# Kernel tuning notes

Measured on AMD Instinct MI355X. Metric: run time of the kernel, lower is better.

Reference implementation:

```python
import jax, jax.numpy as jnp
import numpy as np

S, B, D, N, DH = 1024, 2, 1024, 16, 64  # seq, batch, d_model, n_head, d_head
EPS = 1e-5


def setup_inputs() -> dict:
    key = jax.random.key(0)
    k0, k1, k2, k3 = jax.random.split(key, 4)
    h = jax.random.normal(k0, (S, B, D), dtype=jnp.float32)
    Wq = jax.random.normal(k1, (N * DH, D), dtype=jnp.float32) * 0.02
    Wkv = jax.random.normal(k2, (2 * N * DH, D), dtype=jnp.float32) * 0.02
    Wo = jax.random.normal(k3, (D, N * DH), dtype=jnp.float32) * 0.02
    gamma = jnp.ones((D,), dtype=jnp.float32)
    beta = jnp.zeros((D,), dtype=jnp.float32)
    return {"h": h, "Wq": Wq, "Wkv": Wkv, "Wo": Wo, "gamma": gamma, "beta": beta}


def reference(h, Wq, Wkv, Wo, gamma, beta):
    scale = 1.0 / np.sqrt(DH).astype(np.float32)
    # projections (torch Linear: x @ W.T), no mems so c == h
    q = (h @ Wq.T).reshape(S, B, N, DH)
    kv = h @ Wkv.T                      # [S,B,2*N*DH]
    k, v = jnp.split(kv, 2, axis=-1)
    k = k.reshape(S, B, N, DH)
    v = v.reshape(S, B, N, DH)
    # full attention scores [i,j,b,n]
    score = jnp.einsum('ibnd,jbnd->ijbn', q, k) * scale
    prob = jax.nn.softmax(score, axis=1)  # softmax over keys j
    # twicing correction (layer_num >= 14): P <- 2P - P @ P per (b,n)
    p = prob.transpose(2, 3, 0, 1)       # [b,n,i,j]
    p = 2.0 * p - jnp.matmul(p, p)
    prob = p.transpose(2, 3, 0, 1)       # back to [i,j,b,n]
    # attention output
    vec = jnp.einsum('ijbn,jbnd->ibnd', prob, v).reshape(S, B, N * DH)
    attn_out = vec @ Wo.T                # [S,B,D]
    # post-LN residual
    x = h + attn_out
    mu = jnp.mean(x, axis=-1, keepdims=True)
    var = jnp.mean(jnp.square(x - mu), axis=-1, keepdims=True)
    return (x - mu) / jnp.sqrt(var + EPS) * gamma + beta
```

## Files before the change

### kernel.cpp

```cpp
#include <hip/hip_runtime.h>

typedef unsigned short u16;
typedef unsigned int u32;
typedef __attribute__((ext_vector_type(8))) short short8;
typedef __attribute__((ext_vector_type(4))) float f32x4;

constexpr int kN = 16, kDH = 64, kD = 1024;
constexpr float kEps = 1e-5f;

__device__ __forceinline__ u16 f2b(float f) {
  u32 u = __float_as_uint(f);
  u += 0x7fffu + ((u >> 16) & 1u);
  return (u16)(u >> 16);
}
__device__ __forceinline__ float b2f(u32 bits) {
  return __uint_as_float(bits << 16);
}

__device__ __forceinline__ void gload16(const u16* g, u16* l) {
  __builtin_amdgcn_global_load_lds(
      (const __attribute__((address_space(1))) void*)g,
      (__attribute__((address_space(3))) void*)l, 16, 0, 0);
}

__device__ __forceinline__ short8 read8sw(const u16* base, int row, int colel) {
  return *(const short8*)(base + (row << 6) + (colel ^ ((row & 7) << 3)));
}

__global__ __launch_bounds__(256) void cvt_all(const float* __restrict__ h,
                                               const float* __restrict__ wq,
                                               const float* __restrict__ wkv,
                                               const float* __restrict__ wo,
                                               u16* __restrict__ hb, u16* __restrict__ wqb,
                                               u16* __restrict__ wkvb, u16* __restrict__ wob) {
  long idx = (long)blockIdx.x * 256 + threadIdx.x;
  const float* in;
  u16* out;
  long base;
  if (idx < 524288L) { in = h; out = hb; base = idx; }
  else if (idx < 786432L) { in = wq; out = wqb; base = idx - 524288L; }
  else if (idx < 1310720L) { in = wkv; out = wkvb; base = idx - 786432L; }
  else { in = wo; out = wob; base = idx - 1310720L; }
  float4 v = *(const float4*)(in + base * 4);
  uint2 o;
  o.x = (u32)f2b(v.x) | ((u32)f2b(v.y) << 16);
  o.y = (u32)f2b(v.z) | ((u32)f2b(v.w) << 16);
  *(uint2*)(out + base * 4) = o;
}

struct GemmParams {
  const u16* A; long ldA;
  const u16* B; long ldB;
  const u16* B2;
  int K;
  u16* ob; float* of; long ldO;
  u16* ob2;
  u16* aux_b16;
};

template <int MODE, int BM, int BN, int WC, int MF, int NF>
__global__ __launch_bounds__(256) void gemm_tile(GemmParams p) {
  __shared__ __align__(16) u16 sm[2][(BM + BN) * 32];
  const u16* A = p.A;
  const int tid = threadIdx.x;
  const int lane = tid & 63;
  const int w = tid >> 6;
  const int wR = w / WC, wC = w % WC;
  const int lr = lane & 15, lk = lane >> 4;
  const int bm0 = blockIdx.y * BM, bn0 = blockIdx.x * BN;
  const int m0 = bm0 + wR * (MF * 16), n0 = bn0 + wC * (NF * 16);
  const u16* B = (MODE == 6 && bn0 >= 1024) ? (p.B2 - 1048576) : p.B;

  f32x4 acc[MF][NF];
#pragma unroll
  for (int i = 0; i < MF; ++i)
#pragma unroll
    for (int j = 0; j < NF; ++j) acc[i][j] = (f32x4){0.f, 0.f, 0.f, 0.f};

  constexpr int ACH = BM * 4;
  constexpr int NCH = (BM + BN) * 4;
  constexpr int NLD = NCH / 256;

  auto stage = [&](int k0, int buf) {
#pragma unroll
    for (int i = 0; i < NLD; ++i) {
      const int cbase = i * 256 + w * 64;
      const int c = cbase + lane;
      const u16* g;
      if (cbase < ACH) {
        g = A + (long)(bm0 + (c >> 2)) * p.ldA + k0 + (c & 3) * 8;
      } else {
        const int cc = c - ACH;
        g = B + (long)(bn0 + (cc >> 2)) * p.ldB + k0 + (cc & 3) * 8;
      }
      gload16(g, &sm[buf][cbase * 8]);
    }
  };

  auto compute = [&](int buf) {
    const u16* As = sm[buf];
    const u16* Bs = sm[buf] + BM * 32;
    short8 af[MF], bf[NF];
#pragma unroll
    for (int mi = 0; mi < MF; ++mi)
      af[mi] = *(const short8*)(As + ((wR * MF + mi) * 16 + lr) * 32 + lk * 8);
#pragma unroll
    for (int ni = 0; ni < NF; ++ni)
      bf[ni] = *(const short8*)(Bs + ((wC * NF + ni) * 16 + lr) * 32 + lk * 8);
#pragma unroll
    for (int mi = 0; mi < MF; ++mi)
#pragma unroll
      for (int ni = 0; ni < NF; ++ni)
        acc[mi][ni] = __builtin_amdgcn_mfma_f32_16x16x32_bf16(af[mi], bf[ni], acc[mi][ni], 0, 0, 0);
  };

  const int nt = p.K / 32;
  stage(0, 0);
  __syncthreads();
  for (int t = 0; t < nt - 1; ++t) {
    stage((t + 1) * 32, (t & 1) ^ 1);
    compute(t & 1);
    __syncthreads();
  }
  compute((nt - 1) & 1);

#pragma unroll
  for (int mi = 0; mi < MF; ++mi)
#pragma unroll
    for (int ni = 0; ni < NF; ++ni)
#pragma unroll
      for (int r = 0; r < 4; ++r) {
        int row = m0 + mi * 16 + lk * 4 + r;
        int col = n0 + ni * 16 + lr;
        float v = acc[mi][ni][r];
        if constexpr (MODE == 6) {
          if (col < 1024) {
            p.ob[(long)row * 1024 + col] = f2b(v);
          } else if (col < 2048) {
            p.ob2[(long)row * 1024 + (col - 1024)] = f2b(v);
          } else {
            int c = col - 2048, n = c >> 6, dd = c & 63, s = row >> 1, b = row & 1;
            p.aux_b16[(((long)((b * kN + n) * kDH + dd)) << 10) + s] = f2b(v);
          }
        } else {
          p.of[(long)row * p.ldO + col] = v;
        }
      }
}

template <bool SECOND>
__global__ __launch_bounds__(256) void flash_tw(const u16* __restrict__ qp,
                                                const u16* __restrict__ kp,
                                                const u16* __restrict__ bp,
                                                float* __restrict__ linv_g,
                                                u16* __restrict__ outp) {
  __shared__ __align__(16) u16 Qs[64 * 64];
  __shared__ __align__(16) u16 Ks[2][64 * 64];
  __shared__ __align__(16) u16 Bs[2][64 * 64];
  __shared__ __align__(16) u16 Ss[64 * 64];
  const int z = blockIdx.y;
  const int qb0 = blockIdx.x * 64;
  const int tid = threadIdx.x, lane = tid & 63, w = tid >> 6;
  const int lr = lane & 15, lk = lane >> 4;
  const int wR = w >> 1, wC = w & 1;

#pragma unroll
  for (int i = 0; i < 2; ++i) {
    int c = i * 256 + w * 64 + lane;
    int row = c >> 3, col = (c & 7) ^ (row & 7);
    gload16(qp + (long)(qb0 + row) * 2048 + z * 64 + col * 8, Qs + c * 8);
  }
  auto stageKB = [&](int j, int buf) {
#pragma unroll
    for (int i = 0; i < 2; ++i) {
      int c = i * 256 + w * 64 + lane;
      int row = c >> 3, col = (c & 7) ^ (row & 7);
      gload16(kp + (long)(j * 64 + row) * 2048 + z * 64 + col * 8, Ks[buf] + c * 8);
      gload16(bp + (long)z * 65536 + (long)row * 1024 + j * 64 + col * 8, Bs[buf] + c * 8);
    }
  };
  stageKB(0, 0);
  __syncthreads();

  short8 qf[2][2];
#pragma unroll
  for (int qi = 0; qi < 2; ++qi)
#pragma unroll
    for (int kk = 0; kk < 2; ++kk)
      qf[qi][kk] = read8sw(Qs, wC * 32 + qi * 16 + lr, kk * 32 + lk * 8);

  f32x4 acc[2][2];
#pragma unroll
  for (int i = 0; i < 2; ++i)
#pragma unroll
    for (int j = 0; j < 2; ++j) acc[i][j] = (f32x4){0.f, 0.f, 0.f, 0.f};
  float lsum[2] = {0.f, 0.f};

  for (int j = 0; j < 16; ++j) {
    const int cur = j & 1;
    if (j < 15) stageKB(j + 1, cur ^ 1);
    f32x4 st[2][2];
#pragma unroll
    for (int a = 0; a < 2; ++a)
#pragma unroll
      for (int b = 0; b < 2; ++b) st[a][b] = (f32x4){0.f, 0.f, 0.f, 0.f};
#pragma unroll
    for (int kk = 0; kk < 2; ++kk)
#pragma unroll
      for (int ki = 0; ki < 2; ++ki) {
        short8 kf = read8sw(Ks[cur], wR * 32 + ki * 16 + lr, kk * 32 + lk * 8);
#pragma unroll
        for (int qi = 0; qi < 2; ++qi)
          st[ki][qi] = __builtin_amdgcn_mfma_f32_16x16x32_bf16(kf, qf[qi][kk], st[ki][qi], 0, 0, 0);
      }
#pragma unroll
    for (int ki = 0; ki < 2; ++ki)
#pragma unroll
      for (int qi = 0; qi < 2; ++qi) {
        float e0 = __expf(st[ki][qi][0] * 0.125f);
        float e1 = __expf(st[ki][qi][1] * 0.125f);
        float e2 = __expf(st[ki][qi][2] * 0.125f);
        float e3 = __expf(st[ki][qi][3] * 0.125f);
        if (!SECOND) lsum[qi] += e0 + e1 + e2 + e3;
        int q = wC * 32 + qi * 16 + lr;
        int k0 = wR * 32 + ki * 16 + lk * 4;
        uint2 pk;
        pk.x = (u32)f2b(e0) | ((u32)f2b(e1) << 16);
        pk.y = (u32)f2b(e2) | ((u32)f2b(e3) << 16);
        *(uint2*)(Ss + ((q << 6) + (k0 ^ ((q & 7) << 3)))) = pk;
      }
    __syncthreads();
#pragma unroll
    for (int kk = 0; kk < 2; ++kk) {
      short8 sf0 = read8sw(Ss, wR * 32 + lr, kk * 32 + lk * 8);
      short8 sf1 = read8sw(Ss, wR * 32 + 16 + lr, kk * 32 + lk * 8);
      short8 bf0 = read8sw(Bs[cur], wC * 32 + lr, kk * 32 + lk * 8);
      short8 bf1 = read8sw(Bs[cur], wC * 32 + 16 + lr, kk * 32 + lk * 8);
      acc[0][0] = __builtin_amdgcn_mfma_f32_16x16x32_bf16(sf0, bf0, acc[0][0], 0, 0, 0);
      acc[0][1] = __builtin_amdgcn_mfma_f32_16x16x32_bf16(sf0, bf1, acc[0][1], 0, 0, 0);
      acc[1][0] = __builtin_amdgcn_mfma_f32_16x16x32_bf16(sf1, bf0, acc[1][0], 0, 0, 0);
      acc[1][1] = __builtin_amdgcn_mfma_f32_16x16x32_bf16(sf1, bf1, acc[1][1], 0, 0, 0);
    }
    __syncthreads();
  }

  float* lred = (float*)Ss;
  if (!SECOND) {
#pragma unroll
    for (int qi = 0; qi < 2; ++qi) {
      lsum[qi] += __shfl_xor(lsum[qi], 16);
      lsum[qi] += __shfl_xor(lsum[qi], 32);
      if (lane < 16) lred[wR * 64 + wC * 32 + qi * 16 + lr] = lsum[qi];
    }
    __syncthreads();
    if (tid < 64) {
      float inv = 1.f / (lred[tid] + lred[64 + tid]);
      lred[128 + tid] = inv;
      linv_g[(long)z * 1024 + qb0 + tid] = inv;
    }
    __syncthreads();
  }

#pragma unroll
  for (int qi = 0; qi < 2; ++qi) {
    const int q0 = wR * 32 + qi * 16 + lk * 4;
#pragma unroll
    for (int ni = 0; ni < 2; ++ni) {
      const int d = wC * 32 + ni * 16 + lr;
      if (!SECOND) {
        const float* linv_s = lred + 128;
        u32 lo = (u32)f2b(acc[qi][ni][0] * linv_s[q0]) | ((u32)f2b(acc[qi][ni][1] * linv_s[q0 + 1]) << 16);
        u32 hi = (u32)f2b(acc[qi][ni][2] * linv_s[q0 + 2]) | ((u32)f2b(acc[qi][ni][3] * linv_s[q0 + 3]) << 16);
        uint2 pk; pk.x = lo; pk.y = hi;
        *(uint2*)(outp + (long)z * 65536 + (long)d * 1024 + qb0 + q0) = pk;
      } else {
        float4 l4 = *(const float4*)(linv_g + (long)z * 1024 + qb0 + q0);
        uint2 ut = *(const uint2*)(bp + (long)z * 65536 + (long)d * 1024 + qb0 + q0);
        float u0 = b2f(ut.x & 0xffffu), u1 = b2f(ut.x >> 16);
        float u2 = b2f(ut.y & 0xffffu), u3 = b2f(ut.y >> 16);
        long ob = (long)(qb0 + q0) * 2048 + z * 64 + d;
        outp[ob]        = f2b(2.f * u0 - acc[qi][ni][0] * l4.x);
        outp[ob + 2048] = f2b(2.f * u1 - acc[qi][ni][1] * l4.y);
        outp[ob + 4096] = f2b(2.f * u2 - acc[qi][ni][2] * l4.z);
        outp[ob + 6144] = f2b(2.f * u3 - acc[qi][ni][3] * l4.w);
      }
    }
  }
}

__global__ __launch_bounds__(256) void resid_ln(const float* __restrict__ h,
                                                const float* __restrict__ attn,
                                                const float* __restrict__ gamma,
                                                const float* __restrict__ beta,
                                                float* __restrict__ out) {
  __shared__ float rs[4], rs2[4];
  const long row = blockIdx.x;
  const int t = threadIdx.x;
  long base = (row << 10) + t * 4;
  float4 hv = *(const float4*)(h + base);
  float4 av = *(const float4*)(attn + base);
  float x0 = hv.x + av.x, x1 = hv.y + av.y, x2 = hv.z + av.z, x3 = hv.w + av.w;
  float s = x0 + x1 + x2 + x3;
  float s2 = x0 * x0 + x1 * x1 + x2 * x2 + x3 * x3;
  for (int o = 32; o; o >>= 1) { s += __shfl_xor(s, o); s2 += __shfl_xor(s2, o); }
  int wid = t >> 6;
  if ((t & 63) == 0) { rs[wid] = s; rs2[wid] = s2; }
  __syncthreads();
  s = rs[0] + rs[1] + rs[2] + rs[3];
  s2 = rs2[0] + rs2[1] + rs2[2] + rs2[3];
  float mean = s * (1.f / 1024.f);
  float var = s2 * (1.f / 1024.f) - mean * mean;
  float rstd = rsqrtf(var + kEps);
  int d = t * 4;
  float4 g = *(const float4*)(gamma + d);
  float4 bt = *(const float4*)(beta + d);
  float4 o_;
  o_.x = (x0 - mean) * rstd * g.x + bt.x;
  o_.y = (x1 - mean) * rstd * g.y + bt.y;
  o_.z = (x2 - mean) * rstd * g.z + bt.z;
  o_.w = (x3 - mean) * rstd * g.w + bt.w;
  *(float4*)(out + base) = o_;
}

extern "C" void kernel_launch(void* const* d_in, const int* in_sizes, int n_in,
                              void* d_out, int out_size, void* d_ws, size_t ws_size,
                              hipStream_t stream) {
  const float* h = (const float*)d_in[0];
  const float* Wq = (const float*)d_in[1];
  const float* Wkv = (const float*)d_in[2];
  const float* Wo = (const float*)d_in[3];
  const float* gamma = (const float*)d_in[4];
  const float* beta = (const float*)d_in[5];
  float* out = (float*)d_out;

  char* ws = (char*)d_ws;
  size_t off = 0;
  auto alloc = [&](size_t bytes) -> void* {
    void* p = ws + off;
    off = (off + bytes + 255) & ~(size_t)255;
    return p;
  };
  u16* hb = (u16*)alloc(2097152ULL * 2);
  u16* Wqb = (u16*)alloc(1048576ULL * 2);
  u16* Wkvb = (u16*)alloc(2097152ULL * 2);
  u16* Wob = (u16*)alloc(1048576ULL * 2);
  u16* qb = (u16*)alloc(2097152ULL * 2);
  u16* kb = (u16*)alloc(2097152ULL * 2);
  u16* vtb = (u16*)alloc(2097152ULL * 2);
  u16* Ut = (u16*)alloc(2097152ULL * 2);
  float* linv = (float*)alloc(32768ULL * 4);
  u16* vecb = (u16*)alloc(2097152ULL * 2);
  float* attn = (float*)alloc(2097152ULL * 4);
  (void)ws_size; (void)n_in; (void)in_sizes; (void)out_size;

  cvt_all<<<6144, 256, 0, stream>>>(h, Wq, Wkv, Wo, hb, Wqb, Wkvb, Wob);

  {
    GemmParams p{};
    p.A = hb; p.ldA = 1024;
    p.B = Wqb; p.ldB = 1024; p.B2 = Wkvb;
    p.K = 1024; p.ob = qb; p.ob2 = kb; p.aux_b16 = vtb;
    gemm_tile<6, 64, 64, 2, 2, 2><<<dim3(48, 32, 1), 256, 0, stream>>>(p);
  }
  flash_tw<false><<<dim3(16, 32), 256, 0, stream>>>(qb, kb, vtb, linv, Ut);
  flash_tw<true><<<dim3(16, 32), 256, 0, stream>>>(qb, kb, Ut, linv, vecb);
  {
    GemmParams p{};
    p.A = vecb; p.ldA = 1024;
    p.B = Wob; p.ldB = 1024;
    p.K = 1024; p.of = attn; p.ldO = 1024;
    gemm_tile<5, 64, 64, 2, 2, 2><<<dim3(16, 32, 1), 256, 0, stream>>>(p);
  }
  resid_ln<<<2048, 256, 0, stream>>>(h, attn, gamma, beta, out);
}
```

Measured before the change: 110.4 us.

## Fuse twicing flash passes via cooperative grid sync; widen GEMM K-tile to 64

After: 188.5 us. +70.7%, slower.

```diff
diff --git a/kernel.cpp b/kernel.cpp
--- a/kernel.cpp
+++ b/kernel.cpp
@@ -1,4 +1,7 @@
 #include <hip/hip_runtime.h>
+#include <hip/hip_cooperative_groups.h>
+
+namespace cg = cooperative_groups;
 
 typedef unsigned short u16;
 typedef unsigned int u32;
@@ -58,76 +61,69 @@
   u16* aux_b16;
 };
 
-template <int MODE, int BM, int BN, int WC, int MF, int NF>
+template <int MODE>
 __global__ __launch_bounds__(256) void gemm_tile(GemmParams p) {
-  __shared__ __align__(16) u16 sm[2][(BM + BN) * 32];
+  __shared__ __align__(16) u16 sm[2][8192];
+  const int tid = threadIdx.x, lane = tid & 63, w = tid >> 6;
+  const int wR = w >> 1, wC = w & 1;
+  const int lr = lane & 15, lk = lane >> 4;
+  const int bm0 = blockIdx.y * 64, bn0 = blockIdx.x * 64;
+  const int m0 = bm0 + wR * 32, n0 = bn0 + wC * 32;
   const u16* A = p.A;
-  const int tid = threadIdx.x;
-  const int lane = tid & 63;
-  const int w = tid >> 6;
-  const int wR = w / WC, wC = w % WC;
-  const int lr = lane & 15, lk = lane >> 4;
-  const int bm0 = blockIdx.y * BM, bn0 = blockIdx.x * BN;
-  const int m0 = bm0 + wR * (MF * 16), n0 = bn0 + wC * (NF * 16);
   const u16* B = (MODE == 6 && bn0 >= 1024) ? (p.B2 - 1048576) : p.B;
 
-  f32x4 acc[MF][NF];
-#pragma unroll
-  for (int i = 0; i < MF; ++i)
-#pragma unroll
-    for (int j = 0; j < NF; ++j) acc[i][j] = (f32x4){0.f, 0.f, 0.f, 0.f};
-
-  constexpr int ACH = BM * 4;
-  constexpr int NCH = (BM + BN) * 4;
-  constexpr int NLD = NCH / 256;
+  f32x4 acc[2][2] = {};
 
   auto stage = [&](int k0, int buf) {
 #pragma unroll
-    for (int i = 0; i < NLD; ++i) {
+    for (int i = 0; i < 4; ++i) {
       const int cbase = i * 256 + w * 64;
       const int c = cbase + lane;
       const u16* g;
-      if (cbase < ACH) {
-        g = A + (long)(bm0 + (c >> 2)) * p.ldA + k0 + (c & 3) * 8;
+      if (cbase < 512) {
+        g = A + (long)(bm0 + (c >> 3)) * p.ldA + k0 + (c & 7) * 8;
       } else {
-        const int cc = c - ACH;
-        g = B + (long)(bn0 + (cc >> 2)) * p.ldB + k0 + (cc & 3) * 8;
+        const int cc = c - 512;
+        g = B + (long)(bn0 + (cc >> 3)) * p.ldB + k0 + (cc & 7) * 8;
       }
-      gload16(g, &sm[buf][cbase * 8]);
+      gload16(g, &sm[buf][(size_t)c * 8]);
     }
   };
 
   auto compute = [&](int buf) {
     const u16* As = sm[buf];
-    const u16* Bs = sm[buf] + BM * 32;
-    short8 af[MF], bf[NF];
-#pragma unroll
-    for (int mi = 0; mi < MF; ++mi)
-      af[mi] = *(const short8*)(As + ((wR * MF + mi) * 16 + lr) * 32 + lk * 8);
-#pragma unroll
-    for (int ni = 0; ni < NF; ++ni)
-      bf[ni] = *(const short8*)(Bs + ((wC * NF + ni) * 16 + lr) * 32 + lk * 8);
-#pragma unroll
-    for (int mi = 0; mi < MF; ++mi)
-#pragma unroll
-      for (int ni = 0; ni < NF; ++ni)
-        acc[mi][ni] = __builtin_amdgcn_mfma_f32_16x16x32_bf16(af[mi], bf[ni], acc[mi][ni], 0, 0, 0);
+    const u16* Bs = sm[buf] + 4096;
+    short8 af[2][2], bf[2][2];
+#pragma unroll
+    for (int mi = 0; mi < 2; ++mi)
+#pragma unroll
+      for (int kk = 0; kk < 2; ++kk) {
+        af[mi][kk] = *(const short8*)(As + ((wR * 2 + mi) * 16 + lr) * 64 + kk * 32 + lk * 8);
+        bf[mi][kk] = *(const short8*)(Bs + ((wC * 2 + mi) * 16 + lr) * 64 + kk * 32 + lk * 8);
+      }
+#pragma unroll
+    for (int kk = 0; kk < 2; ++kk)
+#pragma unroll
+      for (int mi = 0; mi < 2; ++mi)
+#pragma unroll
+        for (int ni = 0; ni < 2; ++ni)
+          acc[mi][ni] = __builtin_amdgcn_mfma_f32_16x16x32_bf16(af[mi][kk], bf[ni][kk], acc[mi][ni], 0, 0, 0);
   };
 
-  const int nt = p.K / 32;
+  const int nt = p.K / 64;
   stage(0, 0);
   __syncthreads();
   for (int t = 0; t < nt - 1; ++t) {
-    stage((t + 1) * 32, (t & 1) ^ 1);
+    stage((t + 1) * 64, (t & 1) ^ 1);
     compute(t & 1);
     __syncthreads();
   }
   compute((nt - 1) & 1);
 
 #pragma unroll
-  for (int mi = 0; mi < MF; ++mi)
-#pragma unroll
-    for (int ni = 0; ni < NF; ++ni)
+  for (int mi = 0; mi < 2; ++mi)
+#pragma unroll
+    for (int ni = 0; ni < 2; ++ni)
 #pragma unroll
       for (int r = 0; r < 4; ++r) {
         int row = m0 + mi * 16 + lk * 4 + r;
@@ -148,35 +144,37 @@
       }
 }
 
-template <bool SECOND>
-__global__ __launch_bounds__(256) void flash_tw(const u16* __restrict__ qp,
-                                                const u16* __restrict__ kp,
-                                                const u16* __restrict__ bp,
-                                                float* __restrict__ linv_g,
-                                                u16* __restrict__ outp) {
-  __shared__ __align__(16) u16 Qs[64 * 64];
-  __shared__ __align__(16) u16 Ks[2][64 * 64];
-  __shared__ __align__(16) u16 Bs[2][64 * 64];
-  __shared__ __align__(16) u16 Ss[64 * 64];
-  const int z = blockIdx.y;
-  const int qb0 = blockIdx.x * 64;
-  const int tid = threadIdx.x, lane = tid & 63, w = tid >> 6;
-  const int lr = lane & 15, lk = lane >> 4;
-  const int wR = w >> 1, wC = w & 1;
-
+struct FlashSmem {
+  alignas(16) u16 Qs[64 * 64];
+  alignas(16) u16 Ks[2][64 * 64];
+  alignas(16) u16 Bs[2][64 * 64];
+  alignas(16) u16 Ss[64 * 64];
+};
+
+__device__ __forceinline__ void flash_stage_q(FlashSmem* sm, const u16* qp, int z, int qb0) {
+  const int tid = threadIdx.x, lane = tid & 63, w = tid >> 6;
 #pragma unroll
   for (int i = 0; i < 2; ++i) {
     int c = i * 256 + w * 64 + lane;
     int row = c >> 3, col = (c & 7) ^ (row & 7);
-    gload16(qp + (long)(qb0 + row) * 2048 + z * 64 + col * 8, Qs + c * 8);
-  }
+    gload16(qp + (long)(qb0 + row) * 2048 + z * 64 + col * 8, sm->Qs + c * 8);
+  }
+}
+
+template <bool DO_LSUM>
+__device__ __forceinline__ void flash_core(FlashSmem* sm, const u16* kp, const u16* bp,
+                                           int z, int qb0, f32x4 acc[2][2], float lsum[2]) {
+  const int tid = threadIdx.x, lane = tid & 63, w = tid >> 6;
+  const int lr = lane & 15, lk = lane >> 4;
+  const int wR = w >> 1, wC = w & 1;
+
   auto stageKB = [&](int j, int buf) {
 #pragma unroll
     for (int i = 0; i < 2; ++i) {
       int c = i * 256 + w * 64 + lane;
       int row = c >> 3, col = (c & 7) ^ (row & 7);
-      gload16(kp + (long)(j * 64 + row) * 2048 + z * 64 + col * 8, Ks[buf] + c * 8);
-      gload16(bp + (long)z * 65536 + (long)row * 1024 + j * 64 + col * 8, Bs[buf] + c * 8);
+      gload16(kp + (long)(j * 64 + row) * 2048 + z * 64 + col * 8, sm->Ks[buf] + c * 8);
+      gload16(bp + (long)z * 65536 + (long)row * 1024 + j * 64 + col * 8, sm->Bs[buf] + c * 8);
     }
   };
   stageKB(0, 0);
@@ -187,14 +185,7 @@
   for (int qi = 0; qi < 2; ++qi)
 #pragma unroll
     for (int kk = 0; kk < 2; ++kk)
-      qf[qi][kk] = read8sw(Qs, wC * 32 + qi * 16 + lr, kk * 32 + lk * 8);
-
-  f32x4 acc[2][2];
-#pragma unroll
-  for (int i = 0; i < 2; ++i)
-#pragma unroll
-    for (int j = 0; j < 2; ++j) acc[i][j] = (f32x4){0.f, 0.f, 0.f, 0.f};
-  float lsum[2] = {0.f, 0.f};
+      qf[qi][kk] = read8sw(sm->Qs, wC * 32 + qi * 16 + lr, kk * 32 + lk * 8);
 
   for (int j = 0; j < 16; ++j) {
     const int cur = j & 1;
@@ -208,7 +199,7 @@
     for (int kk = 0; kk < 2; ++kk)
 #pragma unroll
       for (int ki = 0; ki < 2; ++ki) {
-        short8 kf = read8sw(Ks[cur], wR * 32 + ki * 16 + lr, kk * 32 + lk * 8);
+        short8 kf = read8sw(sm->Ks[cur], wR * 32 + ki * 16 + lr, kk * 32 + lk * 8);
 #pragma unroll
         for (int qi = 0; qi < 2; ++qi)
           st[ki][qi] = __builtin_amdgcn_mfma_f32_16x16x32_bf16(kf, qf[qi][kk], st[ki][qi], 0, 0, 0);
@@ -221,21 +212,21 @@
         float e1 = __expf(st[ki][qi][1] * 0.125f);
         float e2 = __expf(st[ki][qi][2] * 0.125f);
         float e3 = __expf(st[ki][qi][3] * 0.125f);
-        if (!SECOND) lsum[qi] += e0 + e1 + e2 + e3;
+        if (DO_LSUM) lsum[qi] += e0 + e1 + e2 + e3;
         int q = wC * 32 + qi * 16 + lr;
         int k0 = wR * 32 + ki * 16 + lk * 4;
         uint2 pk;
         pk.x = (u32)f2b(e0) | ((u32)f2b(e1) << 16);
         pk.y = (u32)f2b(e2) | ((u32)f2b(e3) << 16);
-        *(uint2*)(Ss + ((q << 6) + (k0 ^ ((q & 7) << 3)))) = pk;
+        *(uint2*)(sm->Ss + ((q << 6) + (k0 ^ ((q & 7) << 3)))) = pk;
       }
     __syncthreads();
 #pragma unroll
     for (int kk = 0; kk < 2; ++kk) {
-      short8 sf0 = read8sw(Ss, wR * 32 + lr, kk * 32 + lk * 8);
-      short8 sf1 = read8sw(Ss, wR * 32 + 16 + lr, kk * 32 + lk * 8);
-      short8 bf0 = read8sw(Bs[cur], wC * 32 + lr, kk * 32 + lk * 8);
-      short8 bf1 = read8sw(Bs[cur], wC * 32 + 16 + lr, kk * 32 + lk * 8);
+      short8 sf0 = read8sw(sm->Ss, wR * 32 + lr, kk * 32 + lk * 8);
+      short8 sf1 = read8sw(sm->Ss, wR * 32 + 16 + lr, kk * 32 + lk * 8);
+      short8 bf0 = read8sw(sm->Bs[cur], wC * 32 + lr, kk * 32 + lk * 8);
+      short8 bf1 = read8sw(sm->Bs[cur], wC * 32 + 16 + lr, kk * 32 + lk * 8);
       acc[0][0] = __builtin_amdgcn_mfma_f32_16x16x32_bf16(sf0, bf0, acc[0][0], 0, 0, 0);
       acc[0][1] = __builtin_amdgcn_mfma_f32_16x16x32_bf16(sf0, bf1, acc[0][1], 0, 0, 0);
       acc[1][0] = __builtin_amdgcn_mfma_f32_16x16x32_bf16(sf1, bf0, acc[1][0], 0, 0, 0);
@@ -243,49 +234,127 @@
     }
     __syncthreads();
   }
-
-  float* lred = (float*)Ss;
-  if (!SECOND) {
-#pragma unroll
-    for (int qi = 0; qi < 2; ++qi) {
-      lsum[qi] += __shfl_xor(lsum[qi], 16);
-      lsum[qi] += __shfl_xor(lsum[qi], 32);
-      if (lane < 16) lred[wR * 64 + wC * 32 + qi * 16 + lr] = lsum[qi];
-    }
-    __syncthreads();
-    if (tid < 64) {
-      float inv = 1.f / (lred[tid] + lred[64 + tid]);
-      lred[128 + tid] = inv;
-      linv_g[(long)z * 1024 + qb0 + tid] = inv;
-    }
-    __syncthreads();
-  }
-
+}
+
+__device__ __forceinline__ void pass1_epilogue(FlashSmem* sm, f32x4 acc[2][2], float lsum[2],
+                                               float lr_[2][4], u16* __restrict__ utp,
+                                               float* __restrict__ linv_g, int z, int qb0) {
+  const int tid = threadIdx.x, lane = tid & 63, w = tid >> 6;
+  const int lr = lane & 15, lk = lane >> 4;
+  const int wR = w >> 1, wC = w & 1;
+  float* lred = (float*)sm->Ss;
+#pragma unroll
+  for (int qi = 0; qi < 2; ++qi) {
+    lsum[qi] += __shfl_xor(lsum[qi], 16);
+    lsum[qi] += __shfl_xor(lsum[qi], 32);
+    if (lane < 16) lred[wR * 64 + wC * 32 + qi * 16 + lr] = lsum[qi];
+  }
+  __syncthreads();
+  if (tid < 64) {
+    float inv = 1.f / (lred[tid] + lred[64 + tid]);
+    lred[128 + tid] = inv;
+    if (linv_g) linv_g[(long)z * 1024 + qb0 + tid] = inv;
+  }
+  __syncthreads();
 #pragma unroll
   for (int qi = 0; qi < 2; ++qi) {
     const int q0 = wR * 32 + qi * 16 + lk * 4;
 #pragma unroll
+    for (int r = 0; r < 4; ++r) lr_[qi][r] = lred[128 + q0 + r];
+#pragma unroll
     for (int ni = 0; ni < 2; ++ni) {
       const int d = wC * 32 + ni * 16 + lr;
-      if (!SECOND) {
-        const float* linv_s = lred + 128;
-        u32 lo = (u32)f2b(acc[qi][ni][0] * linv_s[q0]) | ((u32)f2b(acc[qi][ni][1] * linv_s[q0 + 1]) << 16);
-        u32 hi = (u32)f2b(acc[qi][ni][2] * linv_s[q0 + 2]) | ((u32)f2b(acc[qi][ni][3] * linv_s[q0 + 3]) << 16);
-        uint2 pk; pk.x = lo; pk.y = hi;
-        *(uint2*)(outp + (long)z * 65536 + (long)d * 1024 + qb0 + q0) = pk;
-      } else {
-        float4 l4 = *(const float4*)(linv_g + (long)z * 1024 + qb0 + q0);
-        uint2 ut = *(const uint2*)(bp + (long)z * 65536 + (long)d * 1024 + qb0 + q0);
-        float u0 = b2f(ut.x & 0xffffu), u1 = b2f(ut.x >> 16);
-        float u2 = b2f(ut.y & 0xffffu), u3 = b2f(ut.y >> 16);
-        long ob = (long)(qb0 + q0) * 2048 + z * 64 + d;
-        outp[ob]        = f2b(2.f * u0 - acc[qi][ni][0] * l4.x);
-        outp[ob + 2048] = f2b(2.f * u1 - acc[qi][ni][1] * l4.y);
-        outp[ob + 4096] = f2b(2.f * u2 - acc[qi][ni][2] * l4.z);
-        outp[ob + 6144] = f2b(2.f * u3 - acc[qi][ni][3] * l4.w);
-      }
-    }
-  }
+      uint2 pk;
+      pk.x = (u32)f2b(acc[qi][ni][0] * lr_[qi][0]) | ((u32)f2b(acc[qi][ni][1] * lr_[qi][1]) << 16);
+      pk.y = (u32)f2b(acc[qi][ni][2] * lr_[qi][2]) | ((u32)f2b(acc[qi][ni][3] * lr_[qi][3]) << 16);
+      *(uint2*)(utp + (long)z * 65536 + (long)d * 1024 + qb0 + q0) = pk;
+    }
+  }
+}
+
+__device__ __forceinline__ void pass2_epilogue(f32x4 acc[2][2], const float lr_[2][4],
+                                               const u16* __restrict__ utp,
+                                               u16* __restrict__ vecp, int z, int qb0) {
+  const int tid = threadIdx.x, lane = tid & 63, w = tid >> 6;
+  const int lr = lane & 15, lk = lane >> 4;
+  const int wR = w >> 1, wC = w & 1;
+#pragma unroll
+  for (int qi = 0; qi < 2; ++qi) {
+    const int q0 = wR * 32 + qi * 16 + lk * 4;
+#pragma unroll
+    for (int ni = 0; ni < 2; ++ni) {
+      const int d = wC * 32 + ni * 16 + lr;
+      uint2 ut = *(const uint2*)(utp + (long)z * 65536 + (long)d * 1024 + qb0 + q0);
+      float u0 = b2f(ut.x & 0xffffu), u1 = b2f(ut.x >> 16);
+      float u2 = b2f(ut.y & 0xffffu), u3 = b2f(ut.y >> 16);
+      long ob = (long)(qb0 + q0) * 2048 + z * 64 + d;
+      vecp[ob]        = f2b(2.f * u0 - acc[qi][ni][0] * lr_[qi][0]);
+      vecp[ob + 2048] = f2b(2.f * u1 - acc[qi][ni][1] * lr_[qi][1]);
+      vecp[ob + 4096] = f2b(2.f * u2 - acc[qi][ni][2] * lr_[qi][2]);
+      vecp[ob + 6144] = f2b(2.f * u3 - acc[qi][ni][3] * lr_[qi][3]);
+    }
+  }
+}
+
+__global__ __launch_bounds__(256, 2) void flash_fused(const u16* __restrict__ qp,
+                                                      const u16* __restrict__ kp,
+                                                      const u16* __restrict__ vp,
+                                                      u16* __restrict__ utp,
+                                                      u16* __restrict__ vecp) {
+  __shared__ FlashSmem smem;
+  const int z = blockIdx.y, qb0 = blockIdx.x * 64;
+  flash_stage_q(&smem, qp, z, qb0);
+  f32x4 acc[2][2] = {};
+  float lsum[2] = {0.f, 0.f};
+  flash_core<true>(&smem, kp, vp, z, qb0, acc, lsum);
+  float lr_[2][4];
+  pass1_epilogue(&smem, acc, lsum, lr_, utp, nullptr, z, qb0);
+  cg::this_grid().sync();
+#pragma unroll
+  for (int i = 0; i < 2; ++i)
+#pragma unroll
+    for (int j = 0; j < 2; ++j) acc[i][j] = (f32x4){0.f, 0.f, 0.f, 0.f};
+  flash_core<false>(&smem, kp, utp, z, qb0, acc, lsum);
+  pass2_epilogue(acc, lr_, utp, vecp, z, qb0);
+}
+
+__global__ __launch_bounds__(256, 2) void flash_p1(const u16* __restrict__ qp,
+                                                   const u16* __restrict__ kp,
+                                                   const u16* __restrict__ vp,
+                                                   u16* __restrict__ utp,
+                                                   float* __restrict__ linv_g) {
+  __shared__ FlashSmem smem;
+  const int z = blockIdx.y, qb0 = blockIdx.x * 64;
+  flash_stage_q(&smem, qp, z, qb0);
+  f32x4 acc[2][2] = {};
+  float lsum[2] = {0.f, 0.f};
+  flash_core<true>(&smem, kp, vp, z, qb0, acc, lsum);
+  float lr_[2][4];
+  pass1_epilogue(&smem, acc, lsum, lr_, utp, linv_g, z, qb0);
+}
+
+__global__ __launch_bounds__(256, 2) void flash_p2(const u16* __restrict__ qp,
+                                                   const u16* __restrict__ kp,
+                                                   const u16* __restrict__ utp,
+                                                   const float* __restrict__ linv_g,
+                                                   u16* __restrict__ vecp) {
+  __shared__ FlashSmem smem;
+  const int z = blockIdx.y, qb0 = blockIdx.x * 64;
+  const int tid = threadIdx.x, lane = tid & 63, w = tid >> 6;
+  const int lk = lane >> 4;
+  const int wR = w >> 1;
+  flash_stage_q(&smem, qp, z, qb0);
+  f32x4 acc[2][2] = {};
+  float lsum[2] = {0.f, 0.f};
+  flash_core<false>(&smem, kp, utp, z, qb0, acc, lsum);
+  float lr_[2][4];
+#pragma unroll
+  for (int qi = 0; qi < 2; ++qi) {
+    const int q0 = wR * 32 + qi * 16 + lk * 4;
+    float4 l4 = *(const float4*)(linv_g + (long)z * 1024 + qb0 + q0);
+    lr_[qi][0] = l4.x; lr_[qi][1] = l4.y; lr_[qi][2] = l4.z; lr_[qi][3] = l4.w;
+  }
+  pass2_epilogue(acc, lr_, utp, vecp, z, qb0);
 }
 
 __global__ __launch_bounds__(256) void resid_ln(const float* __restrict__ h,
@@ -360,16 +429,25 @@
     p.A = hb; p.ldA = 1024;
     p.B = Wqb; p.ldB = 1024; p.B2 = Wkvb;
     p.K = 1024; p.ob = qb; p.ob2 = kb; p.aux_b16 = vtb;
-    gemm_tile<6, 64, 64, 2, 2, 2><<<dim3(48, 32, 1), 256, 0, stream>>>(p);
-  }
-  flash_tw<false><<<dim3(16, 32), 256, 0, stream>>>(qb, kb, vtb, linv, Ut);
-  flash_tw<true><<<dim3(16, 32), 256, 0, stream>>>(qb, kb, Ut, linv, vecb);
+    gemm_tile<6><<<dim3(48, 32, 1), 256, 0, stream>>>(p);
+  }
+  {
+    const u16* qp_ = qb; const u16* kp_ = kb; const u16* vp_ = vtb;
+    u16* utp_ = Ut; u16* vecp_ = vecb;
+    void* args[] = {(void*)&qp_, (void*)&kp_, (void*)&vp_, (void*)&utp_, (void*)&vecp_};
+    hipError_t ce = hipLaunchCooperativeKernel((const void*)flash_fused, dim3(16, 32),
+                                               dim3(256), args, 0, stream);
+    if (ce != hipSuccess) {
+      flash_p1<<<dim3(16, 32), 256, 0, stream>>>(qb, kb, vtb, Ut, linv);
+      flash_p2<<<dim3(16, 32), 256, 0, stream>>>(qb, kb, Ut, linv, vecb);
+    }
+  }
   {
     GemmParams p{};
     p.A = vecb; p.ldA = 1024;
     p.B = Wob; p.ldB = 1024;
     p.K = 1024; p.of = attn; p.ldO = 1024;
-    gemm_tile<5, 64, 64, 2, 2, 2><<<dim3(16, 32, 1), 256, 0, stream>>>(p);
+    gemm_tile<5><<<dim3(16, 32, 1), 256, 0, stream>>>(p);
   }
   resid_ln<<<2048, 256, 0, stream>>>(h, attn, gamma, beta, out);
 }
```

## Keep attention probabilities in registers via permuted key layout; widen GEMM K-tile

Applied to the files above, without the earlier changes.

New measurement: 114.8 us. +4.0%, slower.

```diff
diff --git a/kernel.cpp b/kernel.cpp
--- a/kernel.cpp
+++ b/kernel.cpp
@@ -25,6 +25,10 @@
 
 __device__ __forceinline__ short8 read8sw(const u16* base, int row, int colel) {
   return *(const short8*)(base + (row << 6) + (colel ^ ((row & 7) << 3)));
+}
+
+__device__ __forceinline__ int permS(int s) {
+  return (s & ~31) + ((s & 12) << 1) + ((s & 16) >> 2) + (s & 3);
 }
 
 __global__ __launch_bounds__(256) void cvt_all(const float* __restrict__ h,
@@ -58,76 +62,69 @@
   u16* aux_b16;
 };
 
-template <int MODE, int BM, int BN, int WC, int MF, int NF>
+template <int MODE>
 __global__ __launch_bounds__(256) void gemm_tile(GemmParams p) {
-  __shared__ __align__(16) u16 sm[2][(BM + BN) * 32];
+  __shared__ __align__(16) u16 sm[2][8192];
+  const int tid = threadIdx.x, lane = tid & 63, w = tid >> 6;
+  const int wR = w >> 1, wC = w & 1;
+  const int lr = lane & 15, lk = lane >> 4;
+  const int bm0 = blockIdx.y * 64, bn0 = blockIdx.x * 64;
+  const int m0 = bm0 + wR * 32, n0 = bn0 + wC * 32;
   const u16* A = p.A;
-  const int tid = threadIdx.x;
-  const int lane = tid & 63;
-  const int w = tid >> 6;
-  const int wR = w / WC, wC = w % WC;
-  const int lr = lane & 15, lk = lane >> 4;
-  const int bm0 = blockIdx.y * BM, bn0 = blockIdx.x * BN;
-  const int m0 = bm0 + wR * (MF * 16), n0 = bn0 + wC * (NF * 16);
   const u16* B = (MODE == 6 && bn0 >= 1024) ? (p.B2 - 1048576) : p.B;
 
-  f32x4 acc[MF][NF];
-#pragma unroll
-  for (int i = 0; i < MF; ++i)
-#pragma unroll
-    for (int j = 0; j < NF; ++j) acc[i][j] = (f32x4){0.f, 0.f, 0.f, 0.f};
-
-  constexpr int ACH = BM * 4;
-  constexpr int NCH = (BM + BN) * 4;
-  constexpr int NLD = NCH / 256;
+  f32x4 acc[2][2] = {};
 
   auto stage = [&](int k0, int buf) {
 #pragma unroll
-    for (int i = 0; i < NLD; ++i) {
+    for (int i = 0; i < 4; ++i) {
       const int cbase = i * 256 + w * 64;
       const int c = cbase + lane;
       const u16* g;
-      if (cbase < ACH) {
-        g = A + (long)(bm0 + (c >> 2)) * p.ldA + k0 + (c & 3) * 8;
+      if (cbase < 512) {
+        g = A + (long)(bm0 + (c >> 3)) * p.ldA + k0 + (c & 7) * 8;
       } else {
-        const int cc = c - ACH;
-        g = B + (long)(bn0 + (cc >> 2)) * p.ldB + k0 + (cc & 3) * 8;
-      }
-      gload16(g, &sm[buf][cbase * 8]);
+        const int cc = c - 512;
+        g = B + (long)(bn0 + (cc >> 3)) * p.ldB + k0 + (cc & 7) * 8;
+      }
+      gload16(g, &sm[buf][(size_t)c * 8]);
     }
   };
 
   auto compute = [&](int buf) {
     const u16* As = sm[buf];
-    const u16* Bs = sm[buf] + BM * 32;
-    short8 af[MF], bf[NF];
-#pragma unroll
-    for (int mi = 0; mi < MF; ++mi)
-      af[mi] = *(const short8*)(As + ((wR * MF + mi) * 16 + lr) * 32 + lk * 8);
-#pragma unroll
-    for (int ni = 0; ni < NF; ++ni)
-      bf[ni] = *(const short8*)(Bs + ((wC * NF + ni) * 16 + lr) * 32 + lk * 8);
-#pragma unroll
-    for (int mi = 0; mi < MF; ++mi)
-#pragma unroll
-      for (int ni = 0; ni < NF; ++ni)
-        acc[mi][ni] = __builtin_amdgcn_mfma_f32_16x16x32_bf16(af[mi], bf[ni], acc[mi][ni], 0, 0, 0);
+    const u16* Bs = sm[buf] + 4096;
+    short8 af[2][2], bf[2][2];
+#pragma unroll
+    for (int mi = 0; mi < 2; ++mi)
+#pragma unroll
+      for (int kk = 0; kk < 2; ++kk) {
+        af[mi][kk] = *(const short8*)(As + ((wR * 2 + mi) * 16 + lr) * 64 + kk * 32 + lk * 8);
+        bf[mi][kk] = *(const short8*)(Bs + ((wC * 2 + mi) * 16 + lr) * 64 + kk * 32 + lk * 8);
+      }
+#pragma unroll
+    for (int kk = 0; kk < 2; ++kk)
+#pragma unroll
+      for (int mi = 0; mi < 2; ++mi)
+#pragma unroll
+        for (int ni = 0; ni < 2; ++ni)
+          acc[mi][ni] = __builtin_amdgcn_mfma_f32_16x16x32_bf16(af[mi][kk], bf[ni][kk], acc[mi][ni], 0, 0, 0);
   };
 
-  const int nt = p.K / 32;
+  const int nt = p.K / 64;
   stage(0, 0);
   __syncthreads();
   for (int t = 0; t < nt - 1; ++t) {
-    stage((t + 1) * 32, (t & 1) ^ 1);
+    stage((t + 1) * 64, (t & 1) ^ 1);
     compute(t & 1);
     __syncthreads();
   }
   compute((nt - 1) & 1);
 
 #pragma unroll
-  for (int mi = 0; mi < MF; ++mi)
-#pragma unroll
-    for (int ni = 0; ni < NF; ++ni)
+  for (int mi = 0; mi < 2; ++mi)
+#pragma unroll
+    for (int ni = 0; ni < 2; ++ni)
 #pragma unroll
       for (int r = 0; r < 4; ++r) {
         int row = m0 + mi * 16 + lk * 4 + r;
@@ -140,7 +137,7 @@
             p.ob2[(long)row * 1024 + (col - 1024)] = f2b(v);
           } else {
             int c = col - 2048, n = c >> 6, dd = c & 63, s = row >> 1, b = row & 1;
-            p.aux_b16[(((long)((b * kN + n) * kDH + dd)) << 10) + s] = f2b(v);
+            p.aux_b16[(((long)((b * kN + n) * kDH + dd)) << 10) + permS(s)] = f2b(v);
           }
         } else {
           p.of[(long)row * p.ldO + col] = v;
@@ -148,28 +145,20 @@
       }
 }
 
-template <bool SECOND>
-__global__ __launch_bounds__(256) void flash_tw(const u16* __restrict__ qp,
-                                                const u16* __restrict__ kp,
-                                                const u16* __restrict__ bp,
-                                                float* __restrict__ linv_g,
-                                                u16* __restrict__ outp) {
-  __shared__ __align__(16) u16 Qs[64 * 64];
+template <bool PASS1>
+__global__ __launch_bounds__(256, 4) void flash_tw(const u16* __restrict__ qp,
+                                                   const u16* __restrict__ kp,
+                                                   const u16* __restrict__ bp,
+                                                   float* __restrict__ linv_g,
+                                                   u16* __restrict__ outp) {
   __shared__ __align__(16) u16 Ks[2][64 * 64];
   __shared__ __align__(16) u16 Bs[2][64 * 64];
-  __shared__ __align__(16) u16 Ss[64 * 64];
-  const int z = blockIdx.y;
-  const int qb0 = blockIdx.x * 64;
+  __shared__ float lred[64], lrinv[64];
+  const int z = blockIdx.y, qb0 = blockIdx.x * 64;
   const int tid = threadIdx.x, lane = tid & 63, w = tid >> 6;
   const int lr = lane & 15, lk = lane >> 4;
-  const int wR = w >> 1, wC = w & 1;
-
-#pragma unroll
-  for (int i = 0; i < 2; ++i) {
-    int c = i * 256 + w * 64 + lane;
-    int row = c >> 3, col = (c & 7) ^ (row & 7);
-    gload16(qp + (long)(qb0 + row) * 2048 + z * 64 + col * 8, Qs + c * 8);
-  }
+  const int q0 = w * 16;
+
   auto stageKB = [&](int j, int buf) {
 #pragma unroll
     for (int i = 0; i < 2; ++i) {
@@ -179,111 +168,94 @@
       gload16(bp + (long)z * 65536 + (long)row * 1024 + j * 64 + col * 8, Bs[buf] + c * 8);
     }
   };
+
+  short8 qf[2];
+#pragma unroll
+  for (int kk = 0; kk < 2; ++kk)
+    qf[kk] = *(const short8*)(qp + (long)(qb0 + q0 + lr) * 2048 + z * 64 + kk * 32 + lk * 8);
+
   stageKB(0, 0);
   __syncthreads();
 
-  short8 qf[2][2];
-#pragma unroll
-  for (int qi = 0; qi < 2; ++qi)
-#pragma unroll
-    for (int kk = 0; kk < 2; ++kk)
-      qf[qi][kk] = read8sw(Qs, wC * 32 + qi * 16 + lr, kk * 32 + lk * 8);
-
-  f32x4 acc[2][2];
-#pragma unroll
-  for (int i = 0; i < 2; ++i)
-#pragma unroll
-    for (int j = 0; j < 2; ++j) acc[i][j] = (f32x4){0.f, 0.f, 0.f, 0.f};
-  float lsum[2] = {0.f, 0.f};
+  f32x4 acc[4] = {};
+  float lsum = 0.f;
 
   for (int j = 0; j < 16; ++j) {
     const int cur = j & 1;
     if (j < 15) stageKB(j + 1, cur ^ 1);
-    f32x4 st[2][2];
-#pragma unroll
-    for (int a = 0; a < 2; ++a)
-#pragma unroll
-      for (int b = 0; b < 2; ++b) st[a][b] = (f32x4){0.f, 0.f, 0.f, 0.f};
+    f32x4 st[4];
+#pragma unroll
+    for (int kt = 0; kt < 4; ++kt) st[kt] = (f32x4){0.f, 0.f, 0.f, 0.f};
 #pragma unroll
     for (int kk = 0; kk < 2; ++kk)
 #pragma unroll
-      for (int ki = 0; ki < 2; ++ki) {
-        short8 kf = read8sw(Ks[cur], wR * 32 + ki * 16 + lr, kk * 32 + lk * 8);
-#pragma unroll
-        for (int qi = 0; qi < 2; ++qi)
-          st[ki][qi] = __builtin_amdgcn_mfma_f32_16x16x32_bf16(kf, qf[qi][kk], st[ki][qi], 0, 0, 0);
-      }
-#pragma unroll
-    for (int ki = 0; ki < 2; ++ki)
-#pragma unroll
-      for (int qi = 0; qi < 2; ++qi) {
-        float e0 = __expf(st[ki][qi][0] * 0.125f);
-        float e1 = __expf(st[ki][qi][1] * 0.125f);
-        float e2 = __expf(st[ki][qi][2] * 0.125f);
-        float e3 = __expf(st[ki][qi][3] * 0.125f);
-        if (!SECOND) lsum[qi] += e0 + e1 + e2 + e3;
-        int q = wC * 32 + qi * 16 + lr;
-        int k0 = wR * 32 + ki * 16 + lk * 4;
-        uint2 pk;
-        pk.x = (u32)f2b(e0) | ((u32)f2b(e1) << 16);
-        pk.y = (u32)f2b(e2) | ((u32)f2b(e3) << 16);
-        *(uint2*)(Ss + ((q << 6) + (k0 ^ ((q & 7) << 3)))) = pk;
-      }
+      for (int kt = 0; kt < 4; ++kt) {
+        short8 kf = read8sw(Ks[cur], kt * 16 + lr, kk * 32 + lk * 8);
+        st[kt] = __builtin_amdgcn_mfma_f32_16x16x32_bf16(kf, qf[kk], st[kt], 0, 0, 0);
+      }
+    uint2 pk[4];
+#pragma unroll
+    for (int kt = 0; kt < 4; ++kt) {
+      float e0 = __expf(st[kt][0] * 0.125f);
+      float e1 = __expf(st[kt][1] * 0.125f);
+      float e2 = __expf(st[kt][2] * 0.125f);
+      float e3 = __expf(st[kt][3] * 0.125f);
+      if (PASS1) lsum += e0 + e1 + e2 + e3;
+      pk[kt].x = (u32)f2b(e0) | ((u32)f2b(e1) << 16);
+      pk[kt].y = (u32)f2b(e2) | ((u32)f2b(e3) << 16);
+    }
+#pragma unroll
+    for (int kk = 0; kk < 2; ++kk) {
+      union { u32 u[4]; short8 s8; } pa;
+      pa.u[0] = pk[kk * 2].x; pa.u[1] = pk[kk * 2].y;
+      pa.u[2] = pk[kk * 2 + 1].x; pa.u[3] = pk[kk * 2 + 1].y;
+#pragma unroll
+      for (int dt = 0; dt < 4; ++dt) {
+        short8 bf = read8sw(Bs[cur], dt * 16 + lr, kk * 32 + lk * 8);
+        acc[dt] = __builtin_amdgcn_mfma_f32_16x16x32_bf16(pa.s8, bf, acc[dt], 0, 0, 0);
+      }
+    }
     __syncthreads();
-#pragma unroll
-    for (int kk = 0; kk < 2; ++kk) {
-      short8 sf0 = read8sw(Ss, wR * 32 + lr, kk * 32 + lk * 8);
-      short8 sf1 = read8sw(Ss, wR * 32 + 16 + lr, kk * 32 + lk * 8);
-      short8 bf0 = read8sw(Bs[cur], wC * 32 + lr, kk * 32 + lk * 8);
-      short8 bf1 = read8sw(Bs[cur], wC * 32 + 16 + lr, kk * 32 + lk * 8);
-      acc[0][0] = __builtin_amdgcn_mfma_f32_16x16x32_bf16(sf0, bf0, acc[0][0], 0, 0, 0);
-      acc[0][1] = __builtin_amdgcn_mfma_f32_16x16x32_bf16(sf0, bf1, acc[0][1], 0, 0, 0);
-      acc[1][0] = __builtin_amdgcn_mfma_f32_16x16x32_bf16(sf1, bf0, acc[1][0], 0, 0, 0);
-      acc[1][1] = __builtin_amdgcn_mfma_f32_16x16x32_bf16(sf1, bf1, acc[1][1], 0, 0, 0);
-    }
-    __syncthreads();
-  }
-
-  float* lred = (float*)Ss;
-  if (!SECOND) {
-#pragma unroll
-    for (int qi = 0; qi < 2; ++qi) {
-      lsum[qi] += __shfl_xor(lsum[qi], 16);
-      lsum[qi] += __shfl_xor(lsum[qi], 32);
-      if (lane < 16) lred[wR * 64 + wC * 32 + qi * 16 + lr] = lsum[qi];
-    }
+  }
+
+  float iv[4];
+  if (PASS1) {
+    lsum += __shfl_xor(lsum, 16);
+    lsum += __shfl_xor(lsum, 32);
+    if (lane < 16) lred[q0 + lr] = lsum;
     __syncthreads();
     if (tid < 64) {
-      float inv = 1.f / (lred[tid] + lred[64 + tid]);
-      lred[128 + tid] = inv;
-      linv_g[(long)z * 1024 + qb0 + tid] = inv;
+      float v = 1.f / lred[tid];
+      lrinv[tid] = v;
+      linv_g[(long)z * 1024 + qb0 + tid] = v;
     }
     __syncthreads();
-  }
-
-#pragma unroll
-  for (int qi = 0; qi < 2; ++qi) {
-    const int q0 = wR * 32 + qi * 16 + lk * 4;
-#pragma unroll
-    for (int ni = 0; ni < 2; ++ni) {
-      const int d = wC * 32 + ni * 16 + lr;
-      if (!SECOND) {
-        const float* linv_s = lred + 128;
-        u32 lo = (u32)f2b(acc[qi][ni][0] * linv_s[q0]) | ((u32)f2b(acc[qi][ni][1] * linv_s[q0 + 1]) << 16);
-        u32 hi = (u32)f2b(acc[qi][ni][2] * linv_s[q0 + 2]) | ((u32)f2b(acc[qi][ni][3] * linv_s[q0 + 3]) << 16);
-        uint2 pk; pk.x = lo; pk.y = hi;
-        *(uint2*)(outp + (long)z * 65536 + (long)d * 1024 + qb0 + q0) = pk;
-      } else {
-        float4 l4 = *(const float4*)(linv_g + (long)z * 1024 + qb0 + q0);
-        uint2 ut = *(const uint2*)(bp + (long)z * 65536 + (long)d * 1024 + qb0 + q0);
-        float u0 = b2f(ut.x & 0xffffu), u1 = b2f(ut.x >> 16);
-        float u2 = b2f(ut.y & 0xffffu), u3 = b2f(ut.y >> 16);
-        long ob = (long)(qb0 + q0) * 2048 + z * 64 + d;
-        outp[ob]        = f2b(2.f * u0 - acc[qi][ni][0] * l4.x);
-        outp[ob + 2048] = f2b(2.f * u1 - acc[qi][ni][1] * l4.y);
-        outp[ob + 4096] = f2b(2.f * u2 - acc[qi][ni][2] * l4.z);
-        outp[ob + 6144] = f2b(2.f * u3 - acc[qi][ni][3] * l4.w);
-      }
+#pragma unroll
+    for (int r = 0; r < 4; ++r) iv[r] = lrinv[q0 + lk * 4 + r];
+  } else {
+    float4 l4 = *(const float4*)(linv_g + (long)z * 1024 + qb0 + q0 + lk * 4);
+    iv[0] = l4.x; iv[1] = l4.y; iv[2] = l4.z; iv[3] = l4.w;
+  }
+
+  const int sq = qb0 + q0 + lk * 4;
+  const int sp = (sq & ~31) + ((sq & 12) << 1) + ((sq & 16) >> 2);
+#pragma unroll
+  for (int dt = 0; dt < 4; ++dt) {
+    const int d = dt * 16 + lr;
+    if (PASS1) {
+      uint2 o_;
+      o_.x = (u32)f2b(acc[dt][0] * iv[0]) | ((u32)f2b(acc[dt][1] * iv[1]) << 16);
+      o_.y = (u32)f2b(acc[dt][2] * iv[2]) | ((u32)f2b(acc[dt][3] * iv[3]) << 16);
+      *(uint2*)(outp + (long)z * 65536 + (long)d * 1024 + sp) = o_;
+    } else {
+      uint2 ut = *(const uint2*)(bp + (long)z * 65536 + (long)d * 1024 + sp);
+      float u0 = b2f(ut.x & 0xffffu), u1 = b2f(ut.x >> 16);
+      float u2 = b2f(ut.y & 0xffffu), u3 = b2f(ut.y >> 16);
+      long ob = (long)sq * 2048 + z * 64 + d;
+      outp[ob]        = f2b(2.f * u0 - acc[dt][0] * iv[0]);
+      outp[ob + 2048] = f2b(2.f * u1 - acc[dt][1] * iv[1]);
+      outp[ob + 4096] = f2b(2.f * u2 - acc[dt][2] * iv[2]);
+      outp[ob + 6144] = f2b(2.f * u3 - acc[dt][3] * iv[3]);
     }
   }
 }
@@ -360,16 +332,16 @@
     p.A = hb; p.ldA = 1024;
     p.B = Wqb; p.ldB = 1024; p.B2 = Wkvb;
     p.K = 1024; p.ob = qb; p.ob2 = kb; p.aux_b16 = vtb;
-    gemm_tile<6, 64, 64, 2, 2, 2><<<dim3(48, 32, 1), 256, 0, stream>>>(p);
-  }
-  flash_tw<false><<<dim3(16, 32), 256, 0, stream>>>(qb, kb, vtb, linv, Ut);
-  flash_tw<true><<<dim3(16, 32), 256, 0, stream>>>(qb, kb, Ut, linv, vecb);
+    gemm_tile<6><<<dim3(48, 32, 1), 256, 0, stream>>>(p);
+  }
+  flash_tw<true><<<dim3(16, 32), 256, 0, stream>>>(qb, kb, vtb, linv, Ut);
+  flash_tw<false><<<dim3(16, 32), 256, 0, stream>>>(qb, kb, Ut, linv, vecb);
   {
     GemmParams p{};
     p.A = vecb; p.ldA = 1024;
     p.B = Wob; p.ldB = 1024;
     p.K = 1024; p.of = attn; p.ldO = 1024;
-    gemm_tile<5, 64, 64, 2, 2, 2><<<dim3(16, 32, 1), 256, 0, stream>>>(p);
+    gemm_tile<5><<<dim3(16, 32, 1), 256, 0, stream>>>(p);
   }
   resid_ln<<<2048, 256, 0, stream>>>(h, attn, gamma, beta, out);
 }
```
